# Kernel tuning notes

Hardware: AMD Instinct MI355X
Metric: run time of the kernel (lower is better)

Reference implementation:

```python
import jax, jax.numpy as jnp
import numpy as np

MARGIN = 0.2  # contrastive margin
# sim_type_dot = 'MISA': max over image regions, mean over (valid) words


def setup_inputs() -> dict:
    key = jax.random.key(0)
    k1, k2, k3, k4 = jax.random.split(key, 4)
    B, R, W, D = 128, 36, 60, 1024
    im = jax.random.normal(k1, (B, R, D), dtype=jnp.float32)
    s = jax.random.normal(k2, (B, W, D), dtype=jnp.float32)
    x = jax.random.normal(k3, (B, W, D), dtype=jnp.float32)  # unused in math, kept for API fidelity
    s_l = jax.random.randint(k4, (B,), 1, W + 1)  # caption lengths in [1, W]
    return {"im": im, "s": s, "s_l": s_l, "x": x}


def _scores(im, s, s_l):
    # im: (B, R, D) images; s: (B, W, D) captions; s_l: (B,) lengths
    B, W = s.shape[0], s.shape[1]
    # matchmap M[i, j, r, w] = <image j region r, caption i word w>
    M = jnp.einsum('jrd,iwd->ijrw', im, s)
    # MISA: max over regions r, then mean over the n_word valid words of caption i
    M_max = M.max(axis=2)                                   # (i, j, w)
    word_mask = (jnp.arange(W)[None, :] < s_l[:, None]).astype(M.dtype)  # (i, w)
    sims = (M_max * word_mask[:, None, :]).sum(axis=-1) / s_l[:, None].astype(M.dtype)  # (i, j)
    # original layout: scores[image j, caption i]
    return sims.T


def reference(im, s, s_l, x):
    scores = _scores(im, s, s_l)                 # (B, B)
    diag = jnp.diagonal(scores)[:, None]         # (B, 1)
    cost_s = jnp.maximum(MARGIN + scores - diag, 0.0)
    cost_im = jnp.maximum(MARGIN + scores - diag.T, 0.0)
    eye = jnp.eye(scores.shape[0], dtype=bool)
    cost_s = jnp.where(eye, 0.0, cost_s)
    cost_im = jnp.where(eye, 0.0, cost_im)
    return cost_s.sum() + cost_im.sum()
```

## Files before the change

kernel.cpp:

```cpp
#include <hip/hip_runtime.h>
#include <hip/hip_bf16.h>
#include <stdint.h>

#define B_SZ 128
#define R_SZ 36
#define W_SZ 60
#define WP_SZ 64
#define D_SZ 1024
#define MARGIN 0.2f

#define ATILE_B (144 * 64)
#define BTILE_B (256 * 64)
#define BUFB    (ATILE_B + BTILE_B)

typedef __attribute__((ext_vector_type(4))) float f32x4;
typedef __attribute__((ext_vector_type(2))) long longx2;

typedef __attribute__((address_space(3))) unsigned int lds_u32;
typedef const __attribute__((address_space(1))) unsigned int glb_u32;

__device__ __forceinline__ void gload16(const unsigned char* g, unsigned char* l) {
    __builtin_amdgcn_global_load_lds((glb_u32*)g, (lds_u32*)l, 16, 0, 0);
}

__global__ __launch_bounds__(256) void convert_fp8_kernel(
        const float* __restrict__ im, const float* __restrict__ s,
        unsigned char* __restrict__ imb, unsigned char* __restrict__ sb) {
    const int nA = B_SZ * R_SZ * 64;
    const int nB = B_SZ * WP_SZ * 64;
    int i = blockIdx.x * 256 + threadIdx.x;
    const float* srcrow;
    unsigned char* dst;
    int gran;
    if (i < nA) {
        gran = i & 63;
        int row = i >> 6;
        srcrow = im + ((size_t)row << 10);
        dst = imb + (size_t)i * 16;
    } else {
        int i2 = i - nA;
        if (i2 >= nB) return;
        gran = i2 & 63;
        int row = i2 >> 6;
        int j = row >> 6, w = row & 63;
        int ws = w < W_SZ ? w : W_SZ - 1;
        srcrow = s + ((size_t)(j * W_SZ + ws) << 10);
        dst = sb + (size_t)i2 * 16;
    }
    const int kb = gran >> 2, g = gran & 3;
    uint4 o;
    unsigned int* op = (unsigned int*)&o;
#pragma unroll
    for (int q = 0; q < 4; ++q) {
        const int kq = kb * 64 + (q >> 1) * 32 + g * 8 + (q & 1) * 4;
        float4 v = *reinterpret_cast<const float4*>(srcrow + kq);
        int w32 = __builtin_amdgcn_cvt_pk_fp8_f32(v.x, v.y, 0, false);
        w32 = __builtin_amdgcn_cvt_pk_fp8_f32(v.z, v.w, w32, true);
        op[q] = (unsigned int)w32;
    }
    *reinterpret_cast<uint4*>(dst) = o;
}

__global__ __launch_bounds__(512, 4) void scores_kernel(
        const unsigned char* __restrict__ imb,
        const unsigned char* __restrict__ sbp,
        const int* __restrict__ s_l,
        float* __restrict__ S)
{
    __shared__ __align__(16) unsigned char LDS[2 * BUFB];
    __shared__ float red2[8][4];

    const int tid  = threadIdx.x;
    const int wc   = tid >> 6;
    const int lane = tid & 63;
    const int l15  = lane & 15;
    const int kgrp = lane >> 4;

    int bid = blockIdx.x;
    int k8  = bid & 7;
    int w   = bid >> 3;
    int jtg = w >> 5;
    int sw  = w & 31;
    int it  = k8 * 4 + (sw >> 3);
    int jt  = jtg * 8 + (sw & 7);

    const int drow = lane >> 2;
    const int sgr  = ((lane & 3) ^ ((lane >> 3) & 3)) * 16;

    const unsigned char* gsrc[4];
    int ldso[4];
#pragma unroll
    for (int si = 0; si < 4; ++si) {
        int c = wc + si * 8;
        if (c < 9) {
            gsrc[si] = imb + (size_t)(jt * 144 + c * 16 + drow) * 1024 + sgr;
            ldso[si] = c * 1024 + lane * 16;
        } else if (c < 25) {
            int b = c - 9;
            gsrc[si] = sbp + (size_t)(it * 256 + b * 16 + drow) * 1024 + sgr;
            ldso[si] = ATILE_B + b * 1024 + lane * 16;
        }
    }

    const int slot0 = (kgrp ^ ((l15 >> 1) & 3)) * 16;
    const int abase = l15 * 64 + slot0;
    int bbase[2];
#pragma unroll
    for (int cf = 0; cf < 2; ++cf)
        bbase[cf] = ATILE_B + (wc * 32 + cf * 16 + l15) * 64 + slot0;

    f32x4 acc[9][2] = {};

#pragma unroll
    for (int si = 0; si < 4; ++si) {
        int c = wc + si * 8;
        if (c < 25) gload16(gsrc[si], LDS + ldso[si]);
    }
    asm volatile("s_waitcnt vmcnt(0)" ::: "memory");
    __builtin_amdgcn_s_barrier();

#pragma unroll 2
    for (int kt = 0; kt < 16; ++kt) {
        const int cur = kt & 1;
        const unsigned char* base = LDS + cur * BUFB;

        longx2 bfr[2];
#pragma unroll
        for (int cf = 0; cf < 2; ++cf)
            bfr[cf] = *reinterpret_cast<const longx2*>(base + bbase[cf]);

        if (kt < 15) {
            const int ko = (kt + 1) * 64;
            unsigned char* dstb = LDS + (cur ^ 1) * BUFB;
#pragma unroll
            for (int si = 0; si < 4; ++si) {
                int c = wc + si * 8;
                if (c < 25) gload16(gsrc[si] + ko, dstb + ldso[si]);
            }
        }

        __builtin_amdgcn_s_setprio(1);
#pragma unroll
        for (int rf = 0; rf < 9; ++rf) {
            longx2 af = *reinterpret_cast<const longx2*>(base + abase + rf * 1024);
#pragma unroll
            for (int k2 = 0; k2 < 2; ++k2)
#pragma unroll
                for (int cf = 0; cf < 2; ++cf)
                    acc[rf][cf] = __builtin_amdgcn_mfma_f32_16x16x32_fp8_fp8(
                        af[k2], bfr[cf][k2], acc[rf][cf], 0, 0, 0);
        }
        __builtin_amdgcn_s_setprio(0);

        if (kt < 15) {
            asm volatile("s_waitcnt vmcnt(0)" ::: "memory");
            __builtin_amdgcn_s_barrier();
        }
    }

    float mm[2][4];
#pragma unroll
    for (int cf = 0; cf < 2; ++cf)
#pragma unroll
        for (int g = 0; g < 4; ++g) mm[cf][g] = -3.4e38f;

#pragma unroll
    for (int cf = 0; cf < 2; ++cf)
#pragma unroll
        for (int rf = 0; rf < 9; ++rf)
#pragma unroll
            for (int e = 0; e < 4; ++e) {
                const int row0 = rf * 16 + e;
                const int g0 = row0 / 36;
                const int g1 = (row0 + 12) / 36;
                float v = acc[rf][cf][e];
                if (g0 == g1) {
                    mm[cf][g0] = fmaxf(mm[cf][g0], v);
                } else {
                    int lr = row0 + 4 * kgrp;
                    if (lr >= g1 * 36) mm[cf][g1] = fmaxf(mm[cf][g1], v);
                    else               mm[cf][g0] = fmaxf(mm[cf][g0], v);
                }
            }

    const int i_cap = it * 4 + (wc >> 1);
    const int nw = s_l[i_cap];
    float sums[4];
#pragma unroll
    for (int g = 0; g < 4; ++g) {
        float sg = 0.0f;
#pragma unroll
        for (int cf = 0; cf < 2; ++cf) {
            float m = mm[cf][g];
            m = fmaxf(m, __shfl_xor(m, 16));
            m = fmaxf(m, __shfl_xor(m, 32));
            int wv = (wc & 1) * 32 + cf * 16 + l15;
            if (wv < nw) sg += m;
        }
        sg += __shfl_xor(sg, 1);
        sg += __shfl_xor(sg, 2);
        sg += __shfl_xor(sg, 4);
        sg += __shfl_xor(sg, 8);
        sums[g] = sg;
    }
    if (lane == 0) {
#pragma unroll
        for (int g = 0; g < 4; ++g) red2[wc][g] = sums[g];
    }
    __syncthreads();
    if ((wc & 1) == 0 && lane == 0) {
        const float inv = 1.0f / (float)nw;
#pragma unroll
        for (int g = 0; g < 4; ++g) {
            int j_img = jt * 4 + g;
            S[j_img * B_SZ + i_cap] = (red2[wc][g] + red2[wc + 1][g]) * inv;
        }
    }
}

__global__ __launch_bounds__(1024) void loss_kernel(
        const float* __restrict__ S, float* __restrict__ out) {
    __shared__ float diag[B_SZ];
    __shared__ float red[1024];
    int t = threadIdx.x;
    if (t < B_SZ) diag[t] = S[t * (B_SZ + 1)];
    __syncthreads();
    float acc = 0.0f;
    for (int idx = t; idx < B_SZ * B_SZ; idx += 1024) {
        int a = idx >> 7, b = idx & (B_SZ - 1);
        if (a != b) {
            float v = S[idx];
            acc += fmaxf(MARGIN + v - diag[a], 0.0f)
                 + fmaxf(MARGIN + v - diag[b], 0.0f);
        }
    }
    red[t] = acc;
    __syncthreads();
    for (int s = 512; s > 0; s >>= 1) {
        if (t < s) red[t] += red[t + s];
        __syncthreads();
    }
    if (t == 0) out[0] = red[0];
}

extern "C" void kernel_launch(void* const* d_in, const int* in_sizes, int n_in,
                              void* d_out, int out_size, void* d_ws, size_t ws_size,
                              hipStream_t stream) {
    const float* im  = (const float*)d_in[0];
    const float* s   = (const float*)d_in[1];
    const int*   s_l = (const int*)d_in[2];

    const int n_im = B_SZ * R_SZ * D_SZ;
    const int n_s  = B_SZ * WP_SZ * D_SZ;

    unsigned char* imb = (unsigned char*)d_ws;
    unsigned char* sb  = imb + n_im;
    float* S = (float*)(sb + n_s);

    const int ngran = (n_im + n_s) / 16;
    convert_fp8_kernel<<<(ngran + 255) / 256, 256, 0, stream>>>(im, s, imb, sb);

    scores_kernel<<<1024, 512, 0, stream>>>(imb, sb, s_l, S);

    loss_kernel<<<1, 1024, 0, stream>>>(S, (float*)d_out);
}
```

Measured before the change: 75.21 us.

## Triple-buffer LDS K-tiles with prefetch distance two and partial vmcnt waits

The scores kernel moves from double to triple buffering of the fp8 A/B tiles in LDS. It prefetches two K-steps ahead and waits only for the oldest batch of global-to-LDS loads (vmcnt 3 or 4, depending on how many loads each wave issues) instead of draining all outstanding loads every iteration. The aim is to hide global load latency behind the MFMA work. In exchange, LDS per block rises by half, which may cut how many blocks fit on each CU, and the tail iteration issues a redundant clamped load.

```diff
diff --git a/kernel.cpp b/kernel.cpp
--- a/kernel.cpp
+++ b/kernel.cpp
@@ -67,7 +67,7 @@
         const int* __restrict__ s_l,
         float* __restrict__ S)
 {
-    __shared__ __align__(16) unsigned char LDS[2 * BUFB];
+    __shared__ __align__(16) unsigned char LDS[3 * BUFB];
     __shared__ float red2[8][4];
 
     const int tid  = threadIdx.x;
@@ -116,29 +116,61 @@
         int c = wc + si * 8;
         if (c < 25) gload16(gsrc[si], LDS + ldso[si]);
     }
-    asm volatile("s_waitcnt vmcnt(0)" ::: "memory");
+#pragma unroll
+    for (int si = 0; si < 4; ++si) {
+        int c = wc + si * 8;
+        if (c < 25) gload16(gsrc[si] + 64, LDS + BUFB + ldso[si]);
+    }
+    if (wc == 0) { asm volatile("s_waitcnt vmcnt(4)" ::: "memory"); }
+    else         { asm volatile("s_waitcnt vmcnt(3)" ::: "memory"); }
     __builtin_amdgcn_s_barrier();
 
-#pragma unroll 2
-    for (int kt = 0; kt < 16; ++kt) {
-        const int cur = kt & 1;
-        const unsigned char* base = LDS + cur * BUFB;
-
+#pragma unroll 1
+    for (int g = 0; g < 5; ++g) {
+#pragma unroll
+        for (int s3 = 0; s3 < 3; ++s3) {
+            const int u = g * 3 + s3;
+            const unsigned char* base = LDS + s3 * BUFB;
+            unsigned char* dstb = LDS + ((s3 + 2) % 3) * BUFB;
+
+            longx2 bfr[2];
+#pragma unroll
+            for (int cf = 0; cf < 2; ++cf)
+                bfr[cf] = *reinterpret_cast<const longx2*>(base + bbase[cf]);
+
+            {
+                const int ko = (u + 2 < 16 ? u + 2 : 15) * 64;
+#pragma unroll
+                for (int si = 0; si < 4; ++si) {
+                    int c = wc + si * 8;
+                    if (c < 25) gload16(gsrc[si] + ko, dstb + ldso[si]);
+                }
+            }
+
+            __builtin_amdgcn_s_setprio(1);
+#pragma unroll
+            for (int rf = 0; rf < 9; ++rf) {
+                longx2 af = *reinterpret_cast<const longx2*>(base + abase + rf * 1024);
+#pragma unroll
+                for (int k2 = 0; k2 < 2; ++k2)
+#pragma unroll
+                    for (int cf = 0; cf < 2; ++cf)
+                        acc[rf][cf] = __builtin_amdgcn_mfma_f32_16x16x32_fp8_fp8(
+                            af[k2], bfr[cf][k2], acc[rf][cf], 0, 0, 0);
+            }
+            __builtin_amdgcn_s_setprio(0);
+
+            if (wc == 0) { asm volatile("s_waitcnt vmcnt(4)" ::: "memory"); }
+            else         { asm volatile("s_waitcnt vmcnt(3)" ::: "memory"); }
+            __builtin_amdgcn_s_barrier();
+        }
+    }
+    {
+        const unsigned char* base = LDS;
         longx2 bfr[2];
 #pragma unroll
         for (int cf = 0; cf < 2; ++cf)
             bfr[cf] = *reinterpret_cast<const longx2*>(base + bbase[cf]);
-
-        if (kt < 15) {
-            const int ko = (kt + 1) * 64;
-            unsigned char* dstb = LDS + (cur ^ 1) * BUFB;
-#pragma unroll
-            for (int si = 0; si < 4; ++si) {
-                int c = wc + si * 8;
-                if (c < 25) gload16(gsrc[si] + ko, dstb + ldso[si]);
-            }
-        }
-
         __builtin_amdgcn_s_setprio(1);
 #pragma unroll
         for (int rf = 0; rf < 9; ++rf) {
@@ -151,11 +183,6 @@
                         af[k2], bfr[cf][k2], acc[rf][cf], 0, 0, 0);
         }
         __builtin_amdgcn_s_setprio(0);
-
-        if (kt < 15) {
-            asm volatile("s_waitcnt vmcnt(0)" ::: "memory");
-            __builtin_amdgcn_s_barrier();
-        }
     }
 
     float mm[2][4];
```

New measurement: 98.39 us. +30.8%, slower.
